# Kernel tuning notes

Measured on AMD Instinct MI355X. Metric: run time of the kernel, lower is better.

The kernel has to match this reference:

```python
import jax, jax.numpy as jnp
import numpy as np
from jax import lax

T = 10.0
DT = 0.1
N_STEPS = 100          # T / dt
NUM_VALS = 10          # number of time-indexed Linear layers
STEPS_PER_SLAB = N_STEPS // NUM_VALS  # 10


def setup_inputs() -> dict:
    key = jax.random.key(0)
    k1, k2, k3 = jax.random.split(key, 3)
    B, D = 1024, 1024
    x = jax.random.normal(k1, (B, D), dtype=jnp.float32)
    # per-time-slab Linear weights/biases (nn.Linear-like scale)
    W = jax.random.normal(k2, (NUM_VALS, D, D), dtype=jnp.float32) * (1.0 / np.sqrt(D))
    b = jax.random.normal(k3, (NUM_VALS, D), dtype=jnp.float32) * 0.01
    return {"x": x, "W": W, "b": b}


def reference(x, W, b):
    # Euler integration of x' = tanh(W_k x + b_k), k = floor(t / (T/num_vals)).
    # Step n has t = n*dt, so k = n // STEPS_PER_SLAB (static schedule).
    ks = jnp.arange(N_STEPS, dtype=jnp.int32) // STEPS_PER_SLAB  # [100]

    def step(h, k):
        # Linear: h @ W_k^T + b_k, then tanh (architecture='inside')
        f = jnp.tanh(h @ W[k].T + b[k])
        h = h + DT * f
        return h, h

    features, traj_tail = lax.scan(step, x, ks)
    # trajectory at linspace(0, T, 101) == Euler grid: prepend initial state
    traj = jnp.concatenate([x[None], traj_tail], axis=0)  # [101, B, D]
    # final_layer=False: forward returns (pred, traj) with pred = features
    return features, traj
```

## Files before the change

### kernel.cpp

```cpp
#include <hip/hip_runtime.h>

#define D 1024
#define DT 0.1f

typedef __attribute__((ext_vector_type(8))) __bf16 bf16x8;
typedef __attribute__((ext_vector_type(4))) float floatx4;

__device__ __forceinline__ unsigned short f2bf(float f) {
  unsigned int u = __builtin_bit_cast(unsigned int, f);
  u = u + 0x7fffu + ((u >> 16) & 1u);
  return (unsigned short)(u >> 16);
}
__device__ __forceinline__ float bf2f(unsigned short b) {
  return __builtin_bit_cast(float, ((unsigned int)b) << 16);
}

__device__ __forceinline__ void gload_lds16(const void* g, void* l) {
  __builtin_amdgcn_global_load_lds(
      (const __attribute__((address_space(1))) void*)g,
      (__attribute__((address_space(3))) void*)l, 16, 0, 0);
}

__device__ __forceinline__ float fast_tanh(float x) {
  float ax = __builtin_fabsf(x);
  float e  = __expf(-2.0f * ax);
  float y  = (1.0f - e) * __builtin_amdgcn_rcpf(1.0f + e);
  return __builtin_copysignf(y, x);
}

__global__ void __launch_bounds__(256) split_kernel(
    const float* __restrict__ src, float* __restrict__ copy_dst,
    unsigned short* __restrict__ hi, unsigned short* __restrict__ lo) {
  const int i = blockIdx.x * blockDim.x + threadIdx.x;
  float4 v = ((const float4*)src)[i];
  if (copy_dst) ((float4*)copy_dst)[i] = v;
  ushort4 h, l;
  h.x = f2bf(v.x); l.x = f2bf(v.x - bf2f(h.x));
  h.y = f2bf(v.y); l.y = f2bf(v.y - bf2f(h.y));
  h.z = f2bf(v.z); l.z = f2bf(v.z - bf2f(h.z));
  h.w = f2bf(v.w); l.w = f2bf(v.w - bf2f(h.w));
  ((ushort4*)hi)[i] = h;
  ((ushort4*)lo)[i] = l;
}

__global__ void __launch_bounds__(512) step_kernel(
    const unsigned short* __restrict__ Ah, const unsigned short* __restrict__ Al,
    const unsigned short* __restrict__ Bh, const unsigned short* __restrict__ Bl,
    const float* __restrict__ bias,
    const float* __restrict__ hprev, float* __restrict__ hnext,
    unsigned short* __restrict__ Nh, unsigned short* __restrict__ Nl,
    float* __restrict__ feat) {
  __shared__ unsigned short lds[3 * 4 * 64 * 64];
  char* ldsb = (char*)lds;

  const int tid  = threadIdx.x;
  const int lane = tid & 63;
  const int wave = tid >> 6;
  const int wr   = wave >> 1;
  const int wc   = wave & 1;

  const int xcd = blockIdx.x & 7;
  const int j8  = blockIdx.x >> 3;
  const int rt  = ((xcd >> 1) << 2) | (j8 >> 3);
  const int ct  = ((xcd & 1) << 3) | (j8 & 7);
  const int row0 = rt << 6;
  const int col0 = ct << 6;

  const int quad = lane >> 4;
  const int l15  = lane & 15;

  const int srow = lane >> 3;
  const int sgrp = (lane & 7) ^ srow;
  const long aoff = (long)(row0 + wave * 8 + srow) * D + sgrp * 8;
  const long boff = (long)(col0 + wave * 8 + srow) * D + sgrp * 8;
  const unsigned short* gAh = Ah + aoff;
  const unsigned short* gAl = Al + aoff;
  const unsigned short* gBh = Bh + boff;
  const unsigned short* gBl = Bl + boff;
  const int sw = wave * 1024;

  const int ecol = col0 + (wc << 5) + l15;
  const int erow = row0 + (wr << 4) + (quad << 2);
  float hp0[4], hp1[4];
#pragma unroll
  for (int r = 0; r < 4; ++r) {
    const long i0 = (long)(erow + r) * D + ecol;
    hp0[r] = hprev[i0];
    hp1[r] = hprev[i0 + 16];
  }
  const float b0 = bias[ecol];
  const float b1 = bias[ecol + 16];

  const int Ra  = (wr << 4) | l15;
  const int Rb0 = (wc << 5) | l15;
  const int Rb1 = Rb0 + 16;
  const int x7  = lane & 7;

  floatx4 acc0 = {0.f, 0.f, 0.f, 0.f};
  floatx4 acc1 = {0.f, 0.f, 0.f, 0.f};

  auto stage = [&](int ck, int bo) {
    const int kk = ck << 6;
    gload_lds16(gAh + kk, ldsb + bo + 0     + sw);
    gload_lds16(gAl + kk, ldsb + bo + 8192  + sw);
    gload_lds16(gBh + kk, ldsb + bo + 16384 + sw);
    gload_lds16(gBl + kk, ldsb + bo + 24576 + sw);
  };

  stage(0, 0);
  stage(1, 32768);

  int cur = 0;
  int nx  = 2;
  for (int c = 0; c < 16; ++c) {
    if (c < 14) stage(c + 2, nx << 15);
    if (c < 14)      asm volatile("s_waitcnt vmcnt(8)" ::: "memory");
    else if (c == 14) asm volatile("s_waitcnt vmcnt(4)" ::: "memory");
    else              asm volatile("s_waitcnt vmcnt(0)" ::: "memory");
    asm volatile("s_barrier" ::: "memory");
    const char* base = ldsb + (cur << 15);
#pragma unroll
    for (int kc = 0; kc < 2; ++kc) {
      const int gs = (((kc << 2) | quad) ^ x7) << 4;
      bf16x8 ah  = *(const bf16x8*)(base + 0     + Ra  * 128 + gs);
      bf16x8 al  = *(const bf16x8*)(base + 8192  + Ra  * 128 + gs);
      bf16x8 bh0 = *(const bf16x8*)(base + 16384 + Rb0 * 128 + gs);
      bf16x8 bl0 = *(const bf16x8*)(base + 24576 + Rb0 * 128 + gs);
      bf16x8 bh1 = *(const bf16x8*)(base + 16384 + Rb1 * 128 + gs);
      bf16x8 bl1 = *(const bf16x8*)(base + 24576 + Rb1 * 128 + gs);
      acc0 = __builtin_amdgcn_mfma_f32_16x16x32_bf16(ah, bh0, acc0, 0, 0, 0);
      acc1 = __builtin_amdgcn_mfma_f32_16x16x32_bf16(ah, bh1, acc1, 0, 0, 0);
      acc0 = __builtin_amdgcn_mfma_f32_16x16x32_bf16(al, bh0, acc0, 0, 0, 0);
      acc1 = __builtin_amdgcn_mfma_f32_16x16x32_bf16(al, bh1, acc1, 0, 0, 0);
      acc0 = __builtin_amdgcn_mfma_f32_16x16x32_bf16(ah, bl0, acc0, 0, 0, 0);
      acc1 = __builtin_amdgcn_mfma_f32_16x16x32_bf16(ah, bl1, acc1, 0, 0, 0);
    }
    asm volatile("s_barrier" ::: "memory");
    cur = (cur == 2) ? 0 : cur + 1;
    nx  = (nx  == 2) ? 0 : nx  + 1;
  }

  const bool wf = (feat != nullptr);
#pragma unroll
  for (int r = 0; r < 4; ++r) {
    const long i0 = (long)(erow + r) * D + ecol;
    {
      float f  = fast_tanh(acc0[r] + b0);
      float hn = hp0[r] + DT * f;
      hnext[i0] = hn;
      unsigned short hb = f2bf(hn);
      Nh[i0] = hb;
      Nl[i0] = f2bf(hn - bf2f(hb));
      if (wf) feat[i0] = hn;
    }
    {
      const long i1 = i0 + 16;
      float f  = fast_tanh(acc1[r] + b1);
      float hn = hp1[r] + DT * f;
      hnext[i1] = hn;
      unsigned short hb = f2bf(hn);
      Nh[i1] = hb;
      Nl[i1] = f2bf(hn - bf2f(hb));
      if (wf) feat[i1] = hn;
    }
  }
}

extern "C" void kernel_launch(void* const* d_in, const int* in_sizes, int n_in,
                              void* d_out, int out_size, void* d_ws, size_t ws_size,
                              hipStream_t stream) {
  const float* x = (const float*)d_in[0];
  const float* W = (const float*)d_in[1];
  const float* b = (const float*)d_in[2];
  float* out  = (float*)d_out;
  float* feat = out;
  float* traj = out + (size_t)D * D;

  const size_t M = (size_t)D * D;
  unsigned short* ws = (unsigned short*)d_ws;
  const int splitBlocks = (int)(M / 4 / 256);

  const bool big = ws_size >= (size_t)48 * 1024 * 1024;

  if (big) {
    unsigned short* wh_all = ws;
    unsigned short* wl_all = wh_all + 10 * M;
    unsigned short* hbuf   = wl_all + 10 * M;
    unsigned short* hh[2] = {hbuf, hbuf + 2 * M};
    unsigned short* hl[2] = {hbuf + M, hbuf + 3 * M};

    split_kernel<<<splitBlocks * 10, 256, 0, stream>>>(W, (float*)nullptr, wh_all, wl_all);
    split_kernel<<<splitBlocks, 256, 0, stream>>>(x, traj, hh[0], hl[0]);

    for (int n = 0; n < 100; ++n) {
      const int k = n / 10;
      step_kernel<<<256, 512, 0, stream>>>(
          hh[n & 1], hl[n & 1], wh_all + (size_t)k * M, wl_all + (size_t)k * M,
          b + (size_t)k * D,
          traj + (size_t)n * M, traj + (size_t)(n + 1) * M,
          hh[(n + 1) & 1], hl[(n + 1) & 1],
          (n == 99) ? feat : nullptr);
    }
  } else {
    unsigned short* wh    = ws;
    unsigned short* wl    = wh + M;
    unsigned short* hbuf  = wl + M;
    unsigned short* hh[2] = {hbuf, hbuf + 2 * M};
    unsigned short* hl[2] = {hbuf + M, hbuf + 3 * M};

    split_kernel<<<splitBlocks, 256, 0, stream>>>(x, traj, hh[0], hl[0]);
    for (int k = 0; k < 10; ++k) {
      split_kernel<<<splitBlocks, 256, 0, stream>>>(W + k * M, (float*)nullptr, wh, wl);
      for (int s = 0; s < 10; ++s) {
        const int n = k * 10 + s;
        step_kernel<<<256, 512, 0, stream>>>(
            hh[n & 1], hl[n & 1], wh, wl, b + (size_t)k * D,
            traj + (size_t)n * M, traj + (size_t)(n + 1) * M,
            hh[(n + 1) & 1], hl[(n + 1) & 1],
            (n == 99) ? feat : nullptr);
      }
    }
  }
}
```

Baseline: 1.492 ms.

## Split K across wave pairs with 32x32 per-wave tiles and LDS reduction

New measurement: 1.579 ms. 1.06x slower.

```diff
diff --git a/kernel.cpp b/kernel.cpp
--- a/kernel.cpp
+++ b/kernel.cpp
@@ -56,8 +56,10 @@
   const int tid  = threadIdx.x;
   const int lane = tid & 63;
   const int wave = tid >> 6;
-  const int wr   = wave >> 1;
-  const int wc   = wave & 1;
+  const int kp   = wave & 1;
+  const int ws   = wave >> 1;
+  const int wr   = ws >> 1;
+  const int wc   = ws & 1;
 
   const int xcd = blockIdx.x & 7;
   const int j8  = blockIdx.x >> 3;
@@ -80,24 +82,31 @@
   const int sw = wave * 1024;
 
   const int ecol = col0 + (wc << 5) + l15;
-  const int erow = row0 + (wr << 4) + (quad << 2);
-  float hp0[4], hp1[4];
+  const int erow = row0 + (wr << 5) + (quad << 2);
+  float hp00[4], hp01[4], hp10[4], hp11[4];
+  float bb0 = 0.f, bb1 = 0.f;
+  if (kp == 0) {
 #pragma unroll
-  for (int r = 0; r < 4; ++r) {
-    const long i0 = (long)(erow + r) * D + ecol;
-    hp0[r] = hprev[i0];
-    hp1[r] = hprev[i0 + 16];
-  }
-  const float b0 = bias[ecol];
-  const float b1 = bias[ecol + 16];
-
-  const int Ra  = (wr << 4) | l15;
+    for (int j = 0; j < 4; ++j) {
+      const long iA = (long)(erow + j) * D + ecol;
+      const long iB = (long)(erow + 16 + j) * D + ecol;
+      hp00[j] = hprev[iA];
+      hp01[j] = hprev[iA + 16];
+      hp10[j] = hprev[iB];
+      hp11[j] = hprev[iB + 16];
+    }
+    bb0 = bias[ecol];
+    bb1 = bias[ecol + 16];
+  }
+
+  const int Ra0 = (wr << 5) | l15;
   const int Rb0 = (wc << 5) | l15;
-  const int Rb1 = Rb0 + 16;
-  const int x7  = lane & 7;
-
-  floatx4 acc0 = {0.f, 0.f, 0.f, 0.f};
-  floatx4 acc1 = {0.f, 0.f, 0.f, 0.f};
+  const int gs  = (((kp << 2) | quad) ^ (lane & 7)) << 4;
+
+  floatx4 acc00 = {0.f, 0.f, 0.f, 0.f};
+  floatx4 acc01 = {0.f, 0.f, 0.f, 0.f};
+  floatx4 acc10 = {0.f, 0.f, 0.f, 0.f};
+  floatx4 acc11 = {0.f, 0.f, 0.f, 0.f};
 
   auto stage = [&](int ck, int bo) {
     const int kk = ck << 6;
@@ -119,51 +128,67 @@
     else              asm volatile("s_waitcnt vmcnt(0)" ::: "memory");
     asm volatile("s_barrier" ::: "memory");
     const char* base = ldsb + (cur << 15);
-#pragma unroll
-    for (int kc = 0; kc < 2; ++kc) {
-      const int gs = (((kc << 2) | quad) ^ x7) << 4;
-      bf16x8 ah  = *(const bf16x8*)(base + 0     + Ra  * 128 + gs);
-      bf16x8 al  = *(const bf16x8*)(base + 8192  + Ra  * 128 + gs);
-      bf16x8 bh0 = *(const bf16x8*)(base + 16384 + Rb0 * 128 + gs);
-      bf16x8 bl0 = *(const bf16x8*)(base + 24576 + Rb0 * 128 + gs);
-      bf16x8 bh1 = *(const bf16x8*)(base + 16384 + Rb1 * 128 + gs);
-      bf16x8 bl1 = *(const bf16x8*)(base + 24576 + Rb1 * 128 + gs);
-      acc0 = __builtin_amdgcn_mfma_f32_16x16x32_bf16(ah, bh0, acc0, 0, 0, 0);
-      acc1 = __builtin_amdgcn_mfma_f32_16x16x32_bf16(ah, bh1, acc1, 0, 0, 0);
-      acc0 = __builtin_amdgcn_mfma_f32_16x16x32_bf16(al, bh0, acc0, 0, 0, 0);
-      acc1 = __builtin_amdgcn_mfma_f32_16x16x32_bf16(al, bh1, acc1, 0, 0, 0);
-      acc0 = __builtin_amdgcn_mfma_f32_16x16x32_bf16(ah, bl0, acc0, 0, 0, 0);
-      acc1 = __builtin_amdgcn_mfma_f32_16x16x32_bf16(ah, bl1, acc1, 0, 0, 0);
-    }
+    bf16x8 ah0 = *(const bf16x8*)(base + 0     + Ra0 * 128        + gs);
+    bf16x8 ah1 = *(const bf16x8*)(base + 0     + (Ra0 + 16) * 128 + gs);
+    bf16x8 al0 = *(const bf16x8*)(base + 8192  + Ra0 * 128        + gs);
+    bf16x8 al1 = *(const bf16x8*)(base + 8192  + (Ra0 + 16) * 128 + gs);
+    bf16x8 bh0 = *(const bf16x8*)(base + 16384 + Rb0 * 128        + gs);
+    bf16x8 bh1 = *(const bf16x8*)(base + 16384 + (Rb0 + 16) * 128 + gs);
+    bf16x8 bl0 = *(const bf16x8*)(base + 24576 + Rb0 * 128        + gs);
+    bf16x8 bl1 = *(const bf16x8*)(base + 24576 + (Rb0 + 16) * 128 + gs);
+    acc00 = __builtin_amdgcn_mfma_f32_16x16x32_bf16(ah0, bh0, acc00, 0, 0, 0);
+    acc01 = __builtin_amdgcn_mfma_f32_16x16x32_bf16(ah0, bh1, acc01, 0, 0, 0);
+    acc10 = __builtin_amdgcn_mfma_f32_16x16x32_bf16(ah1, bh0, acc10, 0, 0, 0);
+    acc11 = __builtin_amdgcn_mfma_f32_16x16x32_bf16(ah1, bh1, acc11, 0, 0, 0);
+    acc00 = __builtin_amdgcn_mfma_f32_16x16x32_bf16(al0, bh0, acc00, 0, 0, 0);
+    acc01 = __builtin_amdgcn_mfma_f32_16x16x32_bf16(al0, bh1, acc01, 0, 0, 0);
+    acc10 = __builtin_amdgcn_mfma_f32_16x16x32_bf16(al1, bh0, acc10, 0, 0, 0);
+    acc11 = __builtin_amdgcn_mfma_f32_16x16x32_bf16(al1, bh1, acc11, 0, 0, 0);
+    acc00 = __builtin_amdgcn_mfma_f32_16x16x32_bf16(ah0, bl0, acc00, 0, 0, 0);
+    acc01 = __builtin_amdgcn_mfma_f32_16x16x32_bf16(ah0, bl1, acc01, 0, 0, 0);
+    acc10 = __builtin_amdgcn_mfma_f32_16x16x32_bf16(ah1, bl0, acc10, 0, 0, 0);
+    acc11 = __builtin_amdgcn_mfma_f32_16x16x32_bf16(ah1, bl1, acc11, 0, 0, 0);
     asm volatile("s_barrier" ::: "memory");
     cur = (cur == 2) ? 0 : cur + 1;
     nx  = (nx  == 2) ? 0 : nx  + 1;
   }
 
+  float* red = (float*)ldsb;
+  const int rbase = (ws << 10) + (lane << 2);
+  if (kp == 1) {
+    *(floatx4*)&red[rbase + 0]   = acc00;
+    *(floatx4*)&red[rbase + 256] = acc01;
+    *(floatx4*)&red[rbase + 512] = acc10;
+    *(floatx4*)&red[rbase + 768] = acc11;
+  }
+  __syncthreads();
+  if (kp == 1) return;
+  acc00 += *(const floatx4*)&red[rbase + 0];
+  acc01 += *(const floatx4*)&red[rbase + 256];
+  acc10 += *(const floatx4*)&red[rbase + 512];
+  acc11 += *(const floatx4*)&red[rbase + 768];
+
   const bool wf = (feat != nullptr);
-#pragma unroll
-  for (int r = 0; r < 4; ++r) {
-    const long i0 = (long)(erow + r) * D + ecol;
-    {
-      float f  = fast_tanh(acc0[r] + b0);
-      float hn = hp0[r] + DT * f;
-      hnext[i0] = hn;
-      unsigned short hb = f2bf(hn);
-      Nh[i0] = hb;
-      Nl[i0] = f2bf(hn - bf2f(hb));
-      if (wf) feat[i0] = hn;
-    }
-    {
-      const long i1 = i0 + 16;
-      float f  = fast_tanh(acc1[r] + b1);
-      float hn = hp1[r] + DT * f;
-      hnext[i1] = hn;
-      unsigned short hb = f2bf(hn);
-      Nh[i1] = hb;
-      Nl[i1] = f2bf(hn - bf2f(hb));
-      if (wf) feat[i1] = hn;
-    }
-  }
+#define EPI(ACC, HP, RR, CC, BC)                                        \
+  do {                                                                  \
+    _Pragma("unroll")                                                   \
+    for (int j = 0; j < 4; ++j) {                                       \
+      const long i = (long)(erow + ((RR) << 4) + j) * D + ecol + ((CC) << 4); \
+      float f  = fast_tanh(ACC[j] + (BC));                              \
+      float hn = HP[j] + DT * f;                                        \
+      hnext[i] = hn;                                                    \
+      unsigned short hb = f2bf(hn);                                     \
+      Nh[i] = hb;                                                       \
+      Nl[i] = f2bf(hn - bf2f(hb));                                      \
+      if (wf) feat[i] = hn;                                             \
+    }                                                                   \
+  } while (0)
+
+  EPI(acc00, hp00, 0, 0, bb0);
+  EPI(acc01, hp01, 0, 1, bb1);
+  EPI(acc10, hp10, 1, 0, bb0);
+  EPI(acc11, hp11, 1, 1, bb1);
+#undef EPI
 }
 
 extern "C" void kernel_launch(void* const* d_in, const int* in_sizes, int n_in,
```
